# Optimization experiments

Hardware: AMD Instinct MI355X
Metric: run time of the kernel (lower is better)

## Reference

```python
import jax, jax.numpy as jnp
import numpy as np

RANK = 16
NUM_STEPS = 10
STEP_SIZE = 1000.0
INIT_SCALE = 1e-3


def _init(k, shape):
    # projection of Dirichlet-like init onto sphere neighborhood: center +- init_scale uniform noise
    center = 1.0 / np.sqrt(shape[-1])
    return (center + (2.0 * INIT_SCALE) * jax.random.uniform(k, shape, dtype=jnp.float32) - INIT_SCALE)


def setup_inputs() -> dict:
    key = jax.random.key(0)
    ks = jax.random.split(key, 5)
    B, H, S, D = 2, 12, 8192, 64
    query = jax.random.normal(ks[0], (B, H, S, D), dtype=jnp.float32)
    key_t = jax.random.normal(ks[1], (B, H, S, D), dtype=jnp.float32)
    value = jax.random.normal(ks[2], (B, H, S, D), dtype=jnp.float32)
    left_params = _init(ks[3], (B, H, S, RANK))
    right_params = _init(ks[4], (B, H, RANK, S))
    return {"query": query, "key": key_t, "value": value,
            "left_params": left_params, "right_params": right_params}


def _unit(x):
    return x / jnp.linalg.norm(x, axis=-1, keepdims=True)


def _grad(lp, rp, q, k, inv_s2):
    # lp: [..., S, r]  rp: [..., r, S]  q,k: [..., S, D]
    ls = _unit(lp)
    rs = _unit(rp)
    L = ls * ls   # left simplex factor  [..., S, r]
    R = rs * rs   # right simplex factor [..., r, S]

    # d_left = (L (R R^T) - Q (K^T R^T)) / S^2   -- contract small dims first, never SxS
    RR = jnp.einsum('...ki,...li->...kl', R, R)          # [r, r]
    KR = jnp.einsum('...ia,...li->...la', k, R)          # [r, D]
    dl = (jnp.einsum('...jk,...kl->...jl', L, RR)
          - jnp.einsum('...ja,...la->...jl', q, KR)) * inv_s2
    dl = dl * 2.0 * ls
    dl = dl - ls * jnp.sum(ls * dl, axis=-1, keepdims=True)   # tangent-space projection
    dl = dl / jnp.linalg.norm(lp, axis=-1, keepdims=True)

    # d_right = ((L^T L) R - (L^T Q) K^T) / S^2
    LL = jnp.einsum('...jk,...jl->...kl', L, L)          # [r, r]
    LQ = jnp.einsum('...jk,...ja->...ka', L, q)          # [r, D]
    dr = (jnp.einsum('...kl,...li->...ki', LL, R)
          - jnp.einsum('...ka,...ia->...ki', LQ, k)) * inv_s2
    dr = dr * 2.0 * rs
    dr = dr - rs * jnp.sum(rs * dr, axis=-1, keepdims=True)
    dr = dr / jnp.linalg.norm(rp, axis=-1, keepdims=True)
    return dl, dr


def _forward(query, key, value, left_params, right_params):
    S = query.shape[-2]
    inv_s2 = jnp.float32(1.0 / (S * S))

    def step(carry, _):
        lp, rp = carry
        dl, dr = _grad(lp, rp, query, key, inv_s2)
        return (lp - STEP_SIZE * dl, rp - STEP_SIZE * dr), None

    (lp, rp), _ = jax.lax.scan(step, (left_params, right_params), None, length=NUM_STEPS)
    left = _unit(lp) ** 2    # [..., S, r]
    right = _unit(rp) ** 2   # [..., r, S]
    # left @ (right @ value) -- rank-bottleneck multiply, O(S*r*D)
    rv = jnp.einsum('...ki,...id->...kd', right, value)
    return jnp.einsum('...jk,...kd->...jd', left, rv)


def reference(query, key, value, left_params, right_params):
    return _forward(query, key, value, left_params, right_params)
```

## Files before the change

### kernel.cpp

```cpp
#include <hip/hip_runtime.h>

#define S_ 8192
#define D_ 64
#define R_ 16
#define BH_ 24

static constexpr float INV_S2 = 1.0f / (8192.0f * 8192.0f);
static constexpr float STEPSZ = 1000.0f;
static constexpr float CC = 2.0f * INV_S2;

#define LP_N (BH_ * S_ * R_)
#define PART_STRIDE 2576
#define PART_N (BH_ * 32 * PART_STRIDE)
#define ACCF_STRIDE 2624
#define ACCF_N (BH_ * ACCF_STRIDE)
#define PART2_STRIDE 1040
#define PART2_N (BH_ * 32 * PART2_STRIDE)

__global__ void __launch_bounds__(256) kA(const float* __restrict__ lp_src,
                                          const float* __restrict__ rp_src,
                                          const float* __restrict__ q,
                                          const float* __restrict__ key,
                                          float* __restrict__ part) {
  const int bh = blockIdx.y, bx = blockIdx.x, t = threadIdx.x;
  const int tc = t & 15, trw = t >> 4, w = t >> 6;
  __shared__ float lds[6144];
  const int j0 = bx * 256;

  {
    size_t base = ((size_t)bh * S_ + j0 + t) * R_;
    const float4* s4 = (const float4*)(lp_src + base);
    float4 a0 = s4[0], a1 = s4[1], a2 = s4[2], a3 = s4[3];
    float n2 = a0.x*a0.x + a0.y*a0.y + a0.z*a0.z + a0.w*a0.w
             + a1.x*a1.x + a1.y*a1.y + a1.z*a1.z + a1.w*a1.w
             + a2.x*a2.x + a2.y*a2.y + a2.z*a2.z + a2.w*a2.w
             + a3.x*a3.x + a3.y*a3.y + a3.z*a3.z + a3.w*a3.w;
    float r2 = 1.0f / n2;
    float4* st = (float4*)(lds + t * 16);
    st[0] = make_float4(a0.x*a0.x*r2, a0.y*a0.y*r2, a0.z*a0.z*r2, a0.w*a0.w*r2);
    st[1] = make_float4(a1.x*a1.x*r2, a1.y*a1.y*r2, a1.z*a1.z*r2, a1.w*a1.w*r2);
    st[2] = make_float4(a2.x*a2.x*r2, a2.y*a2.y*r2, a2.z*a2.z*r2, a2.w*a2.w*r2);
    st[3] = make_float4(a3.x*a3.x*r2, a3.y*a3.y*r2, a3.z*a3.z*r2, a3.w*a3.w*r2);
  }
  __syncthreads();

  float acc[5][16];
#pragma unroll
  for (int u = 0; u < 5; ++u)
#pragma unroll
    for (int l = 0; l < 16; ++l) acc[u][l] = 0.f;

  const float* qb = q + (size_t)bh * S_ * D_;
  for (int it = 0; it < 16; ++it) {
    int jl = trw + (it << 4);
    const float4* L4 = (const float4*)(lds + jl * 16);
    float4 b0 = L4[0], b1 = L4[1], b2 = L4[2], b3 = L4[3];
    float Lv[16] = {b0.x, b0.y, b0.z, b0.w, b1.x, b1.y, b1.z, b1.w,
                    b2.x, b2.y, b2.z, b2.w, b3.x, b3.y, b3.z, b3.w};
    float Lc = lds[jl * 16 + tc];
    float qv[4];
#pragma unroll
    for (int u = 0; u < 4; ++u) qv[u] = qb[(size_t)(j0 + jl) * D_ + tc + (u << 4)];
#pragma unroll
    for (int u = 0; u < 4; ++u)
#pragma unroll
      for (int l = 0; l < 16; ++l) acc[u][l] += Lv[l] * qv[u];
#pragma unroll
    for (int l = 0; l < 16; ++l) acc[4][l] += Lv[l] * Lc;
  }
#pragma unroll
  for (int u = 0; u < 5; ++u)
#pragma unroll
    for (int l = 0; l < 16; ++l) {
      float v = acc[u][l];
      v += __shfl_xor(v, 16);
      v += __shfl_xor(v, 32);
      acc[u][l] = v;
    }
  __syncthreads();
  if ((t & 63) < 16) {
#pragma unroll
    for (int u = 0; u < 5; ++u)
#pragma unroll
      for (int l = 0; l < 16; ++l) lds[w * 1536 + tc * 96 + u * 16 + l] = acc[u][l];
  }
  __syncthreads();
  float* pb = part + (size_t)(bh * 32 + bx) * PART_STRIDE;
#pragma unroll
  for (int r = 0; r < 5; ++r) {
    int o = t + r * 256;
    int sl = o >> 4, c = o & 15;
    pb[o] = lds[c * 96 + sl] + lds[1536 + c * 96 + sl] +
            lds[3072 + c * 96 + sl] + lds[4608 + c * 96 + sl];
  }
  __syncthreads();

  {
    size_t cb = (size_t)bh * R_ * S_ + j0 + t;
    float* st = lds + t * 16;
#pragma unroll
    for (int l = 0; l < 16; ++l) {
      float x = rp_src[cb + (size_t)l * S_];
      st[l] = x * x;
    }
  }
  __syncthreads();

  float accN[16];
#pragma unroll
  for (int u = 0; u < 5; ++u)
#pragma unroll
    for (int l = 0; l < 16; ++l) acc[u][l] = 0.f;
#pragma unroll
  for (int l = 0; l < 16; ++l) accN[l] = 0.f;

  const float* kb = key + (size_t)bh * S_ * D_;
  for (int it = 0; it < 16; ++it) {
    int jl = trw + (it << 4);
    const float4* R4 = (const float4*)(lds + jl * 16);
    float4 b0 = R4[0], b1 = R4[1], b2 = R4[2], b3 = R4[3];
    float rv[16] = {b0.x, b0.y, b0.z, b0.w, b1.x, b1.y, b1.z, b1.w,
                    b2.x, b2.y, b2.z, b2.w, b3.x, b3.y, b3.z, b3.w};
    float rc = lds[jl * 16 + tc];
    float kv[4];
#pragma unroll
    for (int u = 0; u < 4; ++u) kv[u] = kb[(size_t)(j0 + jl) * D_ + tc + (u << 4)];
#pragma unroll
    for (int u = 0; u < 4; ++u)
#pragma unroll
      for (int l = 0; l < 16; ++l) acc[u][l] += rv[l] * kv[u];
#pragma unroll
    for (int l = 0; l < 16; ++l) acc[4][l] += rv[l] * rc;
#pragma unroll
    for (int l = 0; l < 16; ++l) accN[l] += rv[l];
  }
#pragma unroll
  for (int u = 0; u < 5; ++u)
#pragma unroll
    for (int l = 0; l < 16; ++l) {
      float v = acc[u][l];
      v += __shfl_xor(v, 16);
      v += __shfl_xor(v, 32);
      acc[u][l] = v;
    }
#pragma unroll
  for (int l = 0; l < 16; ++l) {
    float v = accN[l];
    v += __shfl_xor(v, 16);
    v += __shfl_xor(v, 32);
    accN[l] = v;
  }
  __syncthreads();
  if ((t & 63) < 16) {
#pragma unroll
    for (int u = 0; u < 5; ++u)
#pragma unroll
      for (int l = 0; l < 16; ++l) lds[w * 1536 + tc * 96 + u * 16 + l] = acc[u][l];
    if (tc == 0) {
#pragma unroll
      for (int l = 0; l < 16; ++l) lds[w * 1536 + 80 + l] = accN[l];
    }
  }
  __syncthreads();
#pragma unroll
  for (int r = 0; r < 5; ++r) {
    int o = t + r * 256;
    int sl = o >> 4, c = o & 15;
    pb[1280 + o] = lds[c * 96 + sl] + lds[1536 + c * 96 + sl] +
                   lds[3072 + c * 96 + sl] + lds[4608 + c * 96 + sl];
  }
  if (t < 16)
    pb[2560 + t] = lds[80 + t] + lds[1536 + 80 + t] + lds[3072 + 80 + t] + lds[4608 + 80 + t];
}

__global__ void __launch_bounds__(256) kB(const float* __restrict__ part,
                                          float* __restrict__ accF) {
  const int bh = blockIdx.x, t = threadIdx.x;
  __shared__ float raw[PART_STRIDE];
  __shared__ float inn[16], srn[16];
  const float* p0 = part + (size_t)bh * 32 * PART_STRIDE;
  for (int v = t; v < PART_STRIDE; v += 256) {
    float s = 0.f;
    const float* p = p0 + v;
#pragma unroll 8
    for (int b = 0; b < 32; ++b) s += p[(size_t)b * PART_STRIDE];
    raw[v] = s;
  }
  __syncthreads();
  if (t < 16) {
    float N = raw[2560 + t];
    inn[t] = 1.0f / N;
    srn[t] = rsqrtf(N);
  }
  __syncthreads();
  float* out = accF + (size_t)bh * ACCF_STRIDE;
  {
    int k = t >> 4, l = t & 15;
    float LLr = raw[(64 + k) * 16 + l];
    out[k * 16 + l] = LLr * CC * inn[l];
    float RRr = raw[1280 + (64 + k) * 16 + l];
    out[1280 + k * 16 + l] = RRr * CC * inn[k] * inn[l];
  }
#pragma unroll
  for (int r = 0; r < 4; ++r) {
    int e = t + r * 256;
    int k = e >> 6, a = e & 63, u = a >> 4, c = a & 15;
    out[256 + e] = raw[(u * 16 + k) * 16 + c] * CC;
  }
#pragma unroll
  for (int r = 0; r < 4; ++r) {
    int e = t + r * 256;
    int a = e >> 4, l = e & 15, u = a >> 4, c = a & 15;
    out[1536 + e] = raw[1280 + (u * 16 + l) * 16 + c] * CC * inn[l];
  }
  if (t < 16) {
    int k = t;
    float s = 0.f;
#pragma unroll
    for (int l = 0; l < 16; ++l)
      s += raw[(64 + k) * 16 + l] * CC * inn[l] * raw[1280 + (64 + k) * 16 + l];
#pragma unroll
    for (int a = 0; a < 64; ++a) {
      int u = a >> 4, c = a & 15;
      s -= raw[(u * 16 + k) * 16 + c] * CC * raw[1280 + (u * 16 + k) * 16 + c];
    }
    float PJ = inn[k] * s;
    out[2560 + t] = 1.0f + STEPSZ * PJ * inn[t];
    out[2576 + t] = STEPSZ * srn[t];
    out[2592 + t] = srn[t];
    out[2608 + t] = inn[t];
  }
}

template <int LAST>
__global__ void __launch_bounds__(256) kStep(const float* __restrict__ accF,
                                             const float* __restrict__ q,
                                             const float* __restrict__ key,
                                             const float* __restrict__ vv,
                                             const float* __restrict__ lp_src,
                                             const float* __restrict__ rp_src,
                                             float* __restrict__ lp_dst,
                                             float* __restrict__ rp_dst,
                                             float* __restrict__ part,
                                             float* __restrict__ part2) {
  const int bh = blockIdx.y, bx = blockIdx.x, t = threadIdx.x;
  const int tc = t & 15, trw = t >> 4, w = t >> 6;
  const int j0 = bx * 256;
  __shared__ float F[1344];
  __shared__ float lds[6144];
  const float* A = accF + (size_t)bh * ACCF_STRIDE;

  if (blockIdx.z == 0) {
    for (int e = t; e < 1280; e += 256) F[e] = A[1280 + e];
    __syncthreads();
    const float4* RR4 = (const float4*)F;
    const float4* KR4 = (const float4*)(F + 256);

    size_t base = ((size_t)bh * S_ + j0 + t) * R_;
    const float4* s4 = (const float4*)(lp_src + base);
    float4 a0 = s4[0], a1 = s4[1], a2 = s4[2], a3 = s4[3];
    float lv[16] = {a0.x, a0.y, a0.z, a0.w, a1.x, a1.y, a1.z, a1.w,
                    a2.x, a2.y, a2.z, a2.w, a3.x, a3.y, a3.z, a3.w};
    float n2 = 0.f;
#pragma unroll
    for (int l = 0; l < 16; ++l) n2 += lv[l] * lv[l];
    float ri = rsqrtf(n2);
    float ls[16], L[16];
#pragma unroll
    for (int l = 0; l < 16; ++l) { ls[l] = lv[l] * ri; L[l] = ls[l] * ls[l]; }
    float dl[16];
#pragma unroll
    for (int l = 0; l < 16; ++l) dl[l] = 0.f;
#pragma unroll
    for (int k = 0; k < 16; ++k) {
      float Lk = L[k];
#pragma unroll
      for (int g = 0; g < 4; ++g) {
        float4 rr = RR4[k * 4 + g];
        dl[4 * g + 0] += Lk * rr.x; dl[4 * g + 1] += Lk * rr.y;
        dl[4 * g + 2] += Lk * rr.z; dl[4 * g + 3] += Lk * rr.w;
      }
    }
    const float4* q4 = (const float4*)(q + ((size_t)bh * S_ + j0 + t) * D_);
#pragma unroll
    for (int a4 = 0; a4 < 16; ++a4) {
      float4 qq = q4[a4];
#pragma unroll
      for (int c = 0; c < 4; ++c) {
        float qa = (c == 0) ? qq.x : (c == 1) ? qq.y : (c == 2) ? qq.z : qq.w;
        int a = a4 * 4 + c;
#pragma unroll
        for (int g = 0; g < 4; ++g) {
          float4 kr = KR4[a * 4 + g];
          dl[4 * g + 0] -= qa * kr.x; dl[4 * g + 1] -= qa * kr.y;
          dl[4 * g + 2] -= qa * kr.z; dl[4 * g + 3] -= qa * kr.w;
        }
      }
    }
    float dot = 0.f;
#pragma unroll
    for (int l = 0; l < 16; ++l) { dl[l] *= ls[l]; dot += ls[l] * dl[l]; }
#pragma unroll
    for (int l = 0; l < 16; ++l)
      lv[l] -= STEPSZ * (dl[l] - ls[l] * dot) * ri;
    float4* d4 = (float4*)(lp_dst + base);
    d4[0] = make_float4(lv[0], lv[1], lv[2], lv[3]);
    d4[1] = make_float4(lv[4], lv[5], lv[6], lv[7]);
    d4[2] = make_float4(lv[8], lv[9], lv[10], lv[11]);
    d4[3] = make_float4(lv[12], lv[13], lv[14], lv[15]);

    if (LAST) return;

    float m2 = 0.f;
#pragma unroll
    for (int l = 0; l < 16; ++l) m2 += lv[l] * lv[l];
    float r2 = 1.0f / m2;
    {
      float4* st = (float4*)(lds + t * 16);
      st[0] = make_float4(lv[0]*lv[0]*r2, lv[1]*lv[1]*r2, lv[2]*lv[2]*r2, lv[3]*lv[3]*r2);
      st[1] = make_float4(lv[4]*lv[4]*r2, lv[5]*lv[5]*r2, lv[6]*lv[6]*r2, lv[7]*lv[7]*r2);
      st[2] = make_float4(lv[8]*lv[8]*r2, lv[9]*lv[9]*r2, lv[10]*lv[10]*r2, lv[11]*lv[11]*r2);
      st[3] = make_float4(lv[12]*lv[12]*r2, lv[13]*lv[13]*r2, lv[14]*lv[14]*r2, lv[15]*lv[15]*r2);
    }
    __syncthreads();
    float acc[5][16];
#pragma unroll
    for (int u = 0; u < 5; ++u)
#pragma unroll
      for (int l = 0; l < 16; ++l) acc[u][l] = 0.f;
    const float* qb = q + (size_t)bh * S_ * D_;
    for (int it = 0; it < 16; ++it) {
      int jl = trw + (it << 4);
      const float4* L4 = (const float4*)(lds + jl * 16);
      float4 b0 = L4[0], b1 = L4[1], b2 = L4[2], b3 = L4[3];
      float Lv[16] = {b0.x, b0.y, b0.z, b0.w, b1.x, b1.y, b1.z, b1.w,
                      b2.x, b2.y, b2.z, b2.w, b3.x, b3.y, b3.z, b3.w};
      float Lc = lds[jl * 16 + tc];
      float qv[4];
#pragma unroll
      for (int u = 0; u < 4; ++u) qv[u] = qb[(size_t)(j0 + jl) * D_ + tc + (u << 4)];
#pragma unroll
      for (int u = 0; u < 4; ++u)
#pragma unroll
        for (int l = 0; l < 16; ++l) acc[u][l] += Lv[l] * qv[u];
#pragma unroll
      for (int l = 0; l < 16; ++l) acc[4][l] += Lv[l] * Lc;
    }
#pragma unroll
    for (int u = 0; u < 5; ++u)
#pragma unroll
      for (int l = 0; l < 16; ++l) {
        float v = acc[u][l];
        v += __shfl_xor(v, 16);
        v += __shfl_xor(v, 32);
        acc[u][l] = v;
      }
    __syncthreads();
    if ((t & 63) < 16) {
#pragma unroll
      for (int u = 0; u < 5; ++u)
#pragma unroll
        for (int l = 0; l < 16; ++l) lds[w * 1536 + tc * 96 + u * 16 + l] = acc[u][l];
    }
    __syncthreads();
    float* pb = part + (size_t)(bh * 32 + bx) * PART_STRIDE;
#pragma unroll
    for (int r = 0; r < 5; ++r) {
      int o = t + r * 256;
      int sl = o >> 4, c = o & 15;
      pb[o] = lds[c * 96 + sl] + lds[1536 + c * 96 + sl] +
              lds[3072 + c * 96 + sl] + lds[4608 + c * 96 + sl];
    }
  } else {
    for (int e = t; e < 1328; e += 256) F[e] = (e < 1280) ? A[e] : A[1280 + e];
    __syncthreads();
    const float4* MLL4 = (const float4*)F;
    const float4* MLQ4 = (const float4*)(F + 256);
    const float* C1 = F + 1280;
    const float* C2 = F + 1296;
    const float* SRN = F + 1312;

    const int i = j0 + t;
    size_t cbase = (size_t)bh * R_ * S_ + i;
    float rv[16], rp2[16];
#pragma unroll
    for (int l = 0; l < 16; ++l) {
      float x = rp_src[cbase + (size_t)l * S_];
      rv[l] = x;
      rp2[l] = x * x;
    }
    float s[16];
#pragma unroll
    for (int k = 0; k < 16; ++k) {
      float acc0 = 0.f;
#pragma unroll
      for (int g = 0; g < 4; ++g) {
        float4 m = MLL4[k * 4 + g];
        acc0 += m.x * rp2[4 * g + 0] + m.y * rp2[4 * g + 1] +
                m.z * rp2[4 * g + 2] + m.w * rp2[4 * g + 3];
      }
      s[k] = acc0;
    }
    const float4* k4 = (const float4*)(key + ((size_t)bh * S_ + i) * D_);
#pragma unroll
    for (int a4 = 0; a4 < 16; ++a4) {
      float4 kk = k4[a4];
#pragma unroll
      for (int k = 0; k < 16; ++k) {
        float4 m = MLQ4[k * 16 + a4];
        s[k] -= m.x * kk.x + m.y * kk.y + m.z * kk.z + m.w * kk.w;
      }
    }
#pragma unroll
    for (int k = 0; k < 16; ++k) {
      float rs = rv[k] * SRN[k];
      float d2 = rs * s[k];
      float nv = C1[k] * rv[k] - C2[k] * d2;
      rp_dst[cbase + (size_t)k * S_] = nv;
      rp2[k] = nv * nv;
    }
    {
      float* st = lds + t * 16;
#pragma unroll
      for (int l = 0; l < 16; ++l) st[l] = rp2[l];
    }
    __syncthreads();
    float acc[5][16], accN[16];
#pragma unroll
    for (int u = 0; u < 5; ++u)
#pragma unroll
      for (int l = 0; l < 16; ++l) acc[u][l] = 0.f;
#pragma unroll
    for (int l = 0; l < 16; ++l) accN[l] = 0.f;
    const float* sb = (LAST ? vv : key) + (size_t)bh * S_ * D_;
    for (int it = 0; it < 16; ++it) {
      int jl = trw + (it << 4);
      const float4* R4 = (const float4*)(lds + jl * 16);
      float4 b0 = R4[0], b1 = R4[1], b2 = R4[2], b3 = R4[3];
      float rw[16] = {b0.x, b0.y, b0.z, b0.w, b1.x, b1.y, b1.z, b1.w,
                      b2.x, b2.y, b2.z, b2.w, b3.x, b3.y, b3.z, b3.w};
      float rc = lds[jl * 16 + tc];
      float kv[4];
#pragma unroll
      for (int u = 0; u < 4; ++u) kv[u] = sb[(size_t)(j0 + jl) * D_ + tc + (u << 4)];
#pragma unroll
      for (int u = 0; u < 4; ++u)
#pragma unroll
        for (int l = 0; l < 16; ++l) acc[u][l] += rw[l] * kv[u];
#pragma unroll
      for (int l = 0; l < 16; ++l) acc[4][l] += rw[l] * rc;
#pragma unroll
      for (int l = 0; l < 16; ++l) accN[l] += rw[l];
    }
#pragma unroll
    for (int u = 0; u < 5; ++u)
#pragma unroll
      for (int l = 0; l < 16; ++l) {
        float v = acc[u][l];
        v += __shfl_xor(v, 16);
        v += __shfl_xor(v, 32);
        acc[u][l] = v;
      }
#pragma unroll
    for (int l = 0; l < 16; ++l) {
      float v = accN[l];
      v += __shfl_xor(v, 16);
      v += __shfl_xor(v, 32);
      accN[l] = v;
    }
    __syncthreads();
    if ((t & 63) < 16) {
#pragma unroll
      for (int u = 0; u < 5; ++u)
#pragma unroll
        for (int l = 0; l < 16; ++l) lds[w * 1536 + tc * 96 + u * 16 + l] = acc[u][l];
      if (tc == 0) {
#pragma unroll
        for (int l = 0; l < 16; ++l) lds[w * 1536 + 80 + l] = accN[l];
      }
    }
    __syncthreads();
    if (!LAST) {
      float* pb = part + (size_t)(bh * 32 + bx) * PART_STRIDE;
#pragma unroll
      for (int r = 0; r < 5; ++r) {
        int o = t + r * 256;
        int sl = o >> 4, c = o & 15;
        pb[1280 + o] = lds[c * 96 + sl] + lds[1536 + c * 96 + sl] +
                       lds[3072 + c * 96 + sl] + lds[4608 + c * 96 + sl];
      }
      if (t < 16)
        pb[2560 + t] = lds[80 + t] + lds[1536 + 80 + t] + lds[3072 + 80 + t] + lds[4608 + 80 + t];
    } else {
      float* pb2 = part2 + (size_t)(bh * 32 + bx) * PART2_STRIDE;
#pragma unroll
      for (int r = 0; r < 4; ++r) {
        int o = t + r * 256;
        int sl = o >> 4, c = o & 15;
        pb2[o] = lds[c * 96 + sl] + lds[1536 + c * 96 + sl] +
                 lds[3072 + c * 96 + sl] + lds[4608 + c * 96 + sl];
      }
      if (t < 16)
        pb2[1024 + t] = lds[80 + t] + lds[1536 + 80 + t] + lds[3072 + 80 + t] + lds[4608 + 80 + t];
    }
  }
}

__global__ void __launch_bounds__(256) kBF(const float* __restrict__ part2,
                                           float* __restrict__ RVs) {
  const int bh = blockIdx.x, t = threadIdx.x;
  __shared__ float raw[PART2_STRIDE];
  __shared__ float inn[16];
  const float* p0 = part2 + (size_t)bh * 32 * PART2_STRIDE;
  for (int v = t; v < PART2_STRIDE; v += 256) {
    float s = 0.f;
    const float* p = p0 + v;
#pragma unroll 8
    for (int b = 0; b < 32; ++b) s += p[(size_t)b * PART2_STRIDE];
    raw[v] = s;
  }
  __syncthreads();
  if (t < 16) inn[t] = 1.0f / raw[1024 + t];
  __syncthreads();
#pragma unroll
  for (int r = 0; r < 4; ++r) {
    int e = t + r * 256;
    int k = e >> 6, d = e & 63, u = d >> 4, c = d & 15;
    RVs[(size_t)bh * 1024 + e] = raw[(u * 16 + k) * 16 + c] * inn[k];
  }
}

__global__ void __launch_bounds__(256) kOut(const float* __restrict__ lp,
                                            const float* __restrict__ RVs,
                                            float* __restrict__ out) {
  const int bh = blockIdx.y, t = threadIdx.x;
  __shared__ float rvs[1024];
#pragma unroll
  for (int r = 0; r < 4; ++r) rvs[t + r * 256] = RVs[(size_t)bh * 1024 + t + r * 256];
  __syncthreads();
  const int j = blockIdx.x * 256 + t;
  size_t base = ((size_t)bh * S_ + j) * R_;
  const float4* lp4 = (const float4*)(lp + base);
  float4 a0 = lp4[0], a1 = lp4[1], a2 = lp4[2], a3 = lp4[3];
  float lv[16] = {a0.x, a0.y, a0.z, a0.w, a1.x, a1.y, a1.z, a1.w,
                  a2.x, a2.y, a2.z, a2.w, a3.x, a3.y, a3.z, a3.w};
  float n2 = 0.f;
#pragma unroll
  for (int l = 0; l < 16; ++l) n2 += lv[l] * lv[l];
  float r2 = 1.0f / n2;
  float L[16];
#pragma unroll
  for (int l = 0; l < 16; ++l) L[l] = lv[l] * lv[l] * r2;
  float o[64];
#pragma unroll
  for (int d = 0; d < 64; ++d) o[d] = 0.f;
  const float4* rv4 = (const float4*)rvs;
#pragma unroll
  for (int k = 0; k < 16; ++k) {
    float Lk = L[k];
#pragma unroll
    for (int d4 = 0; d4 < 16; ++d4) {
      float4 r = rv4[k * 16 + d4];
      o[4 * d4 + 0] += Lk * r.x; o[4 * d4 + 1] += Lk * r.y;
      o[4 * d4 + 2] += Lk * r.z; o[4 * d4 + 3] += Lk * r.w;
    }
  }
  float4* o4 = (float4*)(out + ((size_t)bh * S_ + j) * D_);
#pragma unroll
  for (int d4 = 0; d4 < 16; ++d4)
    o4[d4] = make_float4(o[4 * d4 + 0], o[4 * d4 + 1], o[4 * d4 + 2], o[4 * d4 + 3]);
}

extern "C" void kernel_launch(void* const* d_in, const int* in_sizes, int n_in,
                              void* d_out, int out_size, void* d_ws, size_t ws_size,
                              hipStream_t stream) {
  (void)in_sizes; (void)n_in; (void)out_size; (void)ws_size;
  const float* q = (const float*)d_in[0];
  const float* key = (const float*)d_in[1];
  const float* v = (const float*)d_in[2];
  const float* lp0 = (const float*)d_in[3];
  const float* rp0 = (const float*)d_in[4];
  float* out = (float*)d_out;
  float* ws = (float*)d_ws;

  float* lp = ws;
  float* rp = lp + LP_N;
  float* part = rp + LP_N;
  float* accF = part + PART_N;
  float* part2 = accF + ACCF_N;
  float* RVs = part2 + PART2_N;

  dim3 blk(256);
  dim3 gA(32, BH_);
  dim3 gS(32, BH_, 2);
  kA<<<gA, blk, 0, stream>>>(lp0, rp0, q, key, part);
  for (int s = 0; s < 10; ++s) {
    kB<<<dim3(BH_), blk, 0, stream>>>(part, accF);
    const float* lsrc = (s == 0) ? lp0 : lp;
    const float* rsrc = (s == 0) ? rp0 : rp;
    if (s < 9)
      kStep<0><<<gS, blk, 0, stream>>>(accF, q, key, v, lsrc, rsrc, lp, rp, part, part2);
    else
      kStep<1><<<gS, blk, 0, stream>>>(accF, q, key, v, lsrc, rsrc, lp, rp, part, part2);
  }
  kBF<<<dim3(BH_), blk, 0, stream>>>(part2, RVs);
  kOut<<<gA, blk, 0, stream>>>(lp, RVs, out);
}
```

Before: 957.4 us.

## Store right factor row-major per position and vectorize Q/K loads in step kernel

Folds the initial accumulation kernel into a templated step kernel (mode 0 copies inputs into the workspace) and switches the working right-parameter buffer from [r, S] to a per-position [S, r] layout. Each thread can then load and store its 16 rank values as float4s instead of 16 strided scalar accesses. Q/K/V tiles are now read as one float4 per thread instead of four scalar loads, and the partial-sum layouts in LDS and global memory are reindexed to match. The final step skips the RR accumulation it does not need. In exchange, per-thread accumulator register pressure rises and the reduction indexing becomes more intricate.

```diff
diff --git a/kernel.cpp b/kernel.cpp
--- a/kernel.cpp
+++ b/kernel.cpp
@@ -17,160 +17,333 @@
 #define PART2_STRIDE 1040
 #define PART2_N (BH_ * 32 * PART2_STRIDE)
 
-__global__ void __launch_bounds__(256) kA(const float* __restrict__ lp_src,
-                                          const float* __restrict__ rp_src,
-                                          const float* __restrict__ q,
-                                          const float* __restrict__ key,
-                                          float* __restrict__ part) {
+template <int MODE>
+__global__ void __launch_bounds__(256) kStep(const float* __restrict__ accF,
+                                             const float* __restrict__ q,
+                                             const float* __restrict__ key,
+                                             const float* __restrict__ vv,
+                                             const float* __restrict__ lp_src,
+                                             const float* __restrict__ rp_src,
+                                             float* __restrict__ lp_dst,
+                                             float* __restrict__ rp_dst,
+                                             float* __restrict__ part,
+                                             float* __restrict__ part2) {
   const int bh = blockIdx.y, bx = blockIdx.x, t = threadIdx.x;
-  const int tc = t & 15, trw = t >> 4, w = t >> 6;
-  __shared__ float lds[6144];
+  const int tc = t & 15, trw = t >> 4, w = t >> 6, lane = t & 63;
   const int j0 = bx * 256;
-
-  {
-    size_t base = ((size_t)bh * S_ + j0 + t) * R_;
-    const float4* s4 = (const float4*)(lp_src + base);
-    float4 a0 = s4[0], a1 = s4[1], a2 = s4[2], a3 = s4[3];
-    float n2 = a0.x*a0.x + a0.y*a0.y + a0.z*a0.z + a0.w*a0.w
-             + a1.x*a1.x + a1.y*a1.y + a1.z*a1.z + a1.w*a1.w
-             + a2.x*a2.x + a2.y*a2.y + a2.z*a2.z + a2.w*a2.w
-             + a3.x*a3.x + a3.y*a3.y + a3.z*a3.z + a3.w*a3.w;
-    float r2 = 1.0f / n2;
-    float4* st = (float4*)(lds + t * 16);
-    st[0] = make_float4(a0.x*a0.x*r2, a0.y*a0.y*r2, a0.z*a0.z*r2, a0.w*a0.w*r2);
-    st[1] = make_float4(a1.x*a1.x*r2, a1.y*a1.y*r2, a1.z*a1.z*r2, a1.w*a1.w*r2);
-    st[2] = make_float4(a2.x*a2.x*r2, a2.y*a2.y*r2, a2.z*a2.z*r2, a2.w*a2.w*r2);
-    st[3] = make_float4(a3.x*a3.x*r2, a3.y*a3.y*r2, a3.z*a3.z*r2, a3.w*a3.w*r2);
-  }
-  __syncthreads();
-
-  float acc[5][16];
-#pragma unroll
-  for (int u = 0; u < 5; ++u)
-#pragma unroll
-    for (int l = 0; l < 16; ++l) acc[u][l] = 0.f;
-
-  const float* qb = q + (size_t)bh * S_ * D_;
-  for (int it = 0; it < 16; ++it) {
-    int jl = trw + (it << 4);
-    const float4* L4 = (const float4*)(lds + jl * 16);
-    float4 b0 = L4[0], b1 = L4[1], b2 = L4[2], b3 = L4[3];
-    float Lv[16] = {b0.x, b0.y, b0.z, b0.w, b1.x, b1.y, b1.z, b1.w,
-                    b2.x, b2.y, b2.z, b2.w, b3.x, b3.y, b3.z, b3.w};
-    float Lc = lds[jl * 16 + tc];
-    float qv[4];
-#pragma unroll
-    for (int u = 0; u < 4; ++u) qv[u] = qb[(size_t)(j0 + jl) * D_ + tc + (u << 4)];
-#pragma unroll
-    for (int u = 0; u < 4; ++u)
-#pragma unroll
-      for (int l = 0; l < 16; ++l) acc[u][l] += Lv[l] * qv[u];
-#pragma unroll
-    for (int l = 0; l < 16; ++l) acc[4][l] += Lv[l] * Lc;
-  }
-#pragma unroll
-  for (int u = 0; u < 5; ++u)
+  __shared__ float B[6400];
+  const float* A = accF + (size_t)bh * ACCF_STRIDE;
+
+  if (blockIdx.z == 0) {
+    const size_t base = ((size_t)bh * S_ + j0 + t) * R_;
+    float lv[16];
+    if (MODE >= 1) {
+      for (int e = t; e < 1280; e += 256) B[e] = A[1280 + e];
+      __syncthreads();
+      const float4* RR4 = (const float4*)B;
+      const float4* KR4 = (const float4*)(B + 256);
+      const float4* s4 = (const float4*)(lp_src + base);
+      float4 a0 = s4[0], a1 = s4[1], a2 = s4[2], a3 = s4[3];
+      lv[0]=a0.x; lv[1]=a0.y; lv[2]=a0.z; lv[3]=a0.w;
+      lv[4]=a1.x; lv[5]=a1.y; lv[6]=a1.z; lv[7]=a1.w;
+      lv[8]=a2.x; lv[9]=a2.y; lv[10]=a2.z; lv[11]=a2.w;
+      lv[12]=a3.x; lv[13]=a3.y; lv[14]=a3.z; lv[15]=a3.w;
+      float n2 = 0.f;
+#pragma unroll
+      for (int l = 0; l < 16; ++l) n2 += lv[l] * lv[l];
+      float ri = rsqrtf(n2);
+      float ls[16], L[16];
+#pragma unroll
+      for (int l = 0; l < 16; ++l) { ls[l] = lv[l] * ri; L[l] = ls[l] * ls[l]; }
+      float dl[16];
+#pragma unroll
+      for (int l = 0; l < 16; ++l) dl[l] = 0.f;
+#pragma unroll
+      for (int k = 0; k < 16; ++k) {
+        float Lk = L[k];
+#pragma unroll
+        for (int g = 0; g < 4; ++g) {
+          float4 rr = RR4[k * 4 + g];
+          dl[4*g+0] += Lk * rr.x; dl[4*g+1] += Lk * rr.y;
+          dl[4*g+2] += Lk * rr.z; dl[4*g+3] += Lk * rr.w;
+        }
+      }
+      const float4* q4 = (const float4*)(q + ((size_t)bh * S_ + j0 + t) * D_);
+#pragma unroll
+      for (int a4 = 0; a4 < 16; ++a4) {
+        float4 qq = q4[a4];
+#pragma unroll
+        for (int c = 0; c < 4; ++c) {
+          float qa = (c == 0) ? qq.x : (c == 1) ? qq.y : (c == 2) ? qq.z : qq.w;
+          int a = a4 * 4 + c;
+#pragma unroll
+          for (int g = 0; g < 4; ++g) {
+            float4 kr = KR4[a * 4 + g];
+            dl[4*g+0] -= qa * kr.x; dl[4*g+1] -= qa * kr.y;
+            dl[4*g+2] -= qa * kr.z; dl[4*g+3] -= qa * kr.w;
+          }
+        }
+      }
+      float dot = 0.f;
+#pragma unroll
+      for (int l = 0; l < 16; ++l) { dl[l] *= ls[l]; dot += ls[l] * dl[l]; }
+#pragma unroll
+      for (int l = 0; l < 16; ++l) lv[l] -= STEPSZ * (dl[l] - ls[l] * dot) * ri;
+      float4* d4 = (float4*)(lp_dst + base);
+      d4[0] = make_float4(lv[0], lv[1], lv[2], lv[3]);
+      d4[1] = make_float4(lv[4], lv[5], lv[6], lv[7]);
+      d4[2] = make_float4(lv[8], lv[9], lv[10], lv[11]);
+      d4[3] = make_float4(lv[12], lv[13], lv[14], lv[15]);
+      if (MODE == 2) return;
+      __syncthreads();
+    } else {
+      const float4* s4 = (const float4*)(lp_src + base);
+      float4 a0 = s4[0], a1 = s4[1], a2 = s4[2], a3 = s4[3];
+      lv[0]=a0.x; lv[1]=a0.y; lv[2]=a0.z; lv[3]=a0.w;
+      lv[4]=a1.x; lv[5]=a1.y; lv[6]=a1.z; lv[7]=a1.w;
+      lv[8]=a2.x; lv[9]=a2.y; lv[10]=a2.z; lv[11]=a2.w;
+      lv[12]=a3.x; lv[13]=a3.y; lv[14]=a3.z; lv[15]=a3.w;
+      float4* d4 = (float4*)(lp_dst + base);
+      d4[0] = a0; d4[1] = a1; d4[2] = a2; d4[3] = a3;
+    }
+    {
+      float m2 = 0.f;
+#pragma unroll
+      for (int l = 0; l < 16; ++l) m2 += lv[l] * lv[l];
+      float r2 = 1.0f / m2;
+      float4* st = (float4*)(B + t * 16);
+      st[0] = make_float4(lv[0]*lv[0]*r2, lv[1]*lv[1]*r2, lv[2]*lv[2]*r2, lv[3]*lv[3]*r2);
+      st[1] = make_float4(lv[4]*lv[4]*r2, lv[5]*lv[5]*r2, lv[6]*lv[6]*r2, lv[7]*lv[7]*r2);
+      st[2] = make_float4(lv[8]*lv[8]*r2, lv[9]*lv[9]*r2, lv[10]*lv[10]*r2, lv[11]*lv[11]*r2);
+      st[3] = make_float4(lv[12]*lv[12]*r2, lv[13]*lv[13]*r2, lv[14]*lv[14]*r2, lv[15]*lv[15]*r2);
+    }
+    __syncthreads();
+    float aQ[64], aL[16];
+#pragma unroll
+    for (int e = 0; e < 64; ++e) aQ[e] = 0.f;
+#pragma unroll
+    for (int l = 0; l < 16; ++l) aL[l] = 0.f;
+    const float* qb = q + (size_t)bh * S_ * D_;
+    for (int it = 0; it < 16; ++it) {
+      int jl = trw + (it << 4);
+      const float4* Lw = (const float4*)(B + jl * 16);
+      float4 b0 = Lw[0], b1 = Lw[1], b2 = Lw[2], b3 = Lw[3];
+      float Lv[16] = {b0.x,b0.y,b0.z,b0.w, b1.x,b1.y,b1.z,b1.w,
+                      b2.x,b2.y,b2.z,b2.w, b3.x,b3.y,b3.z,b3.w};
+      float Lc = B[jl * 16 + tc];
+      float4 qq = *(const float4*)(qb + (size_t)(j0 + jl) * D_ + (tc << 2));
+#pragma unroll
+      for (int l = 0; l < 16; ++l) {
+        aQ[l*4+0] += Lv[l] * qq.x; aQ[l*4+1] += Lv[l] * qq.y;
+        aQ[l*4+2] += Lv[l] * qq.z; aQ[l*4+3] += Lv[l] * qq.w;
+        aL[l] += Lv[l] * Lc;
+      }
+    }
+#pragma unroll
+    for (int e = 0; e < 64; ++e) {
+      float v = aQ[e];
+      v += __shfl_xor(v, 16); v += __shfl_xor(v, 32);
+      aQ[e] = v;
+    }
 #pragma unroll
     for (int l = 0; l < 16; ++l) {
-      float v = acc[u][l];
-      v += __shfl_xor(v, 16);
-      v += __shfl_xor(v, 32);
-      acc[u][l] = v;
-    }
-  __syncthreads();
-  if ((t & 63) < 16) {
-#pragma unroll
-    for (int u = 0; u < 5; ++u)
-#pragma unroll
-      for (int l = 0; l < 16; ++l) lds[w * 1536 + tc * 96 + u * 16 + l] = acc[u][l];
-  }
-  __syncthreads();
-  float* pb = part + (size_t)(bh * 32 + bx) * PART_STRIDE;
-#pragma unroll
-  for (int r = 0; r < 5; ++r) {
-    int o = t + r * 256;
-    int sl = o >> 4, c = o & 15;
-    pb[o] = lds[c * 96 + sl] + lds[1536 + c * 96 + sl] +
-            lds[3072 + c * 96 + sl] + lds[4608 + c * 96 + sl];
-  }
-  __syncthreads();
-
-  {
-    size_t cb = (size_t)bh * R_ * S_ + j0 + t;
-    float* st = lds + t * 16;
+      float v = aL[l];
+      v += __shfl_xor(v, 16); v += __shfl_xor(v, 32);
+      aL[l] = v;
+    }
+    __syncthreads();
+    if (lane < 16) {
+      float* rg = B + w * 1600 + tc * 100;
+      float4* rg4 = (float4*)rg;
+#pragma unroll
+      for (int l = 0; l < 16; ++l)
+        rg4[l] = make_float4(aQ[l*4], aQ[l*4+1], aQ[l*4+2], aQ[l*4+3]);
+#pragma unroll
+      for (int l = 0; l < 16; ++l) rg[64 + l] = aL[l];
+    }
+    __syncthreads();
+    float* pb = part + (size_t)(bh * 32 + bx) * PART_STRIDE;
+#pragma unroll
+    for (int r = 0; r < 4; ++r) {
+      int o = t + r * 256;
+      int tcL = o >> 6, sl = o & 63;
+      int idx = tcL * 100 + sl;
+      float s = B[idx] + B[idx + 1600] + B[idx + 3200] + B[idx + 4800];
+      pb[((tcL << 2) + (sl & 3)) * 16 + (sl >> 2)] = s;
+    }
+    {
+      int tcL = t >> 4, l = t & 15;
+      int idx = tcL * 100 + 64 + l;
+      float s = B[idx] + B[idx + 1600] + B[idx + 3200] + B[idx + 4800];
+      pb[1024 + l * 16 + tcL] = s;
+    }
+  } else {
+    const int i = j0 + t;
+    const size_t cb = ((size_t)bh * S_ + i) * R_;
+    float nv[16], rp2[16];
+    if (MODE >= 1) {
+      for (int e = t; e < 1328; e += 256) B[e] = (e < 1280) ? A[e] : A[1280 + e];
+      __syncthreads();
+      const float4* MLL4 = (const float4*)B;
+      const float4* MLQ4 = (const float4*)(B + 256);
+      const float* C1 = B + 1280;
+      const float* C2 = B + 1296;
+      const float* SRN = B + 1312;
+      const float4* r4 = (const float4*)(rp_src + cb);
+      float4 a0 = r4[0], a1 = r4[1], a2 = r4[2], a3 = r4[3];
+      float rv[16] = {a0.x,a0.y,a0.z,a0.w, a1.x,a1.y,a1.z,a1.w,
+                      a2.x,a2.y,a2.z,a2.w, a3.x,a3.y,a3.z,a3.w};
+#pragma unroll
+      for (int l = 0; l < 16; ++l) rp2[l] = rv[l] * rv[l];
+      float s[16];
+#pragma unroll
+      for (int k = 0; k < 16; ++k) {
+        float acc0 = 0.f;
+#pragma unroll
+        for (int g = 0; g < 4; ++g) {
+          float4 m = MLL4[k * 4 + g];
+          acc0 += m.x * rp2[4*g+0] + m.y * rp2[4*g+1] +
+                  m.z * rp2[4*g+2] + m.w * rp2[4*g+3];
+        }
+        s[k] = acc0;
+      }
+      const float4* k4 = (const float4*)(key + ((size_t)bh * S_ + i) * D_);
+#pragma unroll
+      for (int a4 = 0; a4 < 16; ++a4) {
+        float4 kk = k4[a4];
+#pragma unroll
+        for (int k = 0; k < 16; ++k) {
+          float4 m = MLQ4[k * 16 + a4];
+          s[k] -= m.x * kk.x + m.y * kk.y + m.z * kk.z + m.w * kk.w;
+        }
+      }
+#pragma unroll
+      for (int k = 0; k < 16; ++k) {
+        float rs = rv[k] * SRN[k];
+        float d2 = rs * s[k];
+        nv[k] = C1[k] * rv[k] - C2[k] * d2;
+        rp2[k] = nv[k] * nv[k];
+      }
+      float4* d4 = (float4*)(rp_dst + cb);
+      d4[0] = make_float4(nv[0], nv[1], nv[2], nv[3]);
+      d4[1] = make_float4(nv[4], nv[5], nv[6], nv[7]);
+      d4[2] = make_float4(nv[8], nv[9], nv[10], nv[11]);
+      d4[3] = make_float4(nv[12], nv[13], nv[14], nv[15]);
+      __syncthreads();
+    } else {
+      const float* rsrc = rp_src + (size_t)bh * R_ * S_ + i;
+#pragma unroll
+      for (int k = 0; k < 16; ++k) {
+        float x = rsrc[(size_t)k * S_];
+        nv[k] = x;
+        rp2[k] = x * x;
+      }
+      float4* d4 = (float4*)(rp_dst + cb);
+      d4[0] = make_float4(nv[0], nv[1], nv[2], nv[3]);
+      d4[1] = make_float4(nv[4], nv[5], nv[6], nv[7]);
+      d4[2] = make_float4(nv[8], nv[9], nv[10], nv[11]);
+      d4[3] = make_float4(nv[12], nv[13], nv[14], nv[15]);
+    }
+    {
+      float4* st = (float4*)(B + t * 16);
+      st[0] = make_float4(rp2[0], rp2[1], rp2[2], rp2[3]);
+      st[1] = make_float4(rp2[4], rp2[5], rp2[6], rp2[7]);
+      st[2] = make_float4(rp2[8], rp2[9], rp2[10], rp2[11]);
+      st[3] = make_float4(rp2[12], rp2[13], rp2[14], rp2[15]);
+    }
+    __syncthreads();
+    float aQ[64], aR[16], aN[16];
+#pragma unroll
+    for (int e = 0; e < 64; ++e) aQ[e] = 0.f;
+#pragma unroll
+    for (int l = 0; l < 16; ++l) { aR[l] = 0.f; aN[l] = 0.f; }
+    const float* sb = ((MODE == 2) ? vv : key) + (size_t)bh * S_ * D_;
+    for (int it = 0; it < 16; ++it) {
+      int jl = trw + (it << 4);
+      const float4* Rw = (const float4*)(B + jl * 16);
+      float4 b0 = Rw[0], b1 = Rw[1], b2 = Rw[2], b3 = Rw[3];
+      float rw[16] = {b0.x,b0.y,b0.z,b0.w, b1.x,b1.y,b1.z,b1.w,
+                      b2.x,b2.y,b2.z,b2.w, b3.x,b3.y,b3.z,b3.w};
+      float rc = (MODE < 2) ? B[jl * 16 + tc] : 0.f;
+      float4 kk = *(const float4*)(sb + (size_t)(j0 + jl) * D_ + (tc << 2));
+#pragma unroll
+      for (int l = 0; l < 16; ++l) {
+        aQ[l*4+0] += rw[l] * kk.x; aQ[l*4+1] += rw[l] * kk.y;
+        aQ[l*4+2] += rw[l] * kk.z; aQ[l*4+3] += rw[l] * kk.w;
+        if (MODE < 2) aR[l] += rw[l] * rc;
+        aN[l] += rw[l];
+      }
+    }
+#pragma unroll
+    for (int e = 0; e < 64; ++e) {
+      float v = aQ[e];
+      v += __shfl_xor(v, 16); v += __shfl_xor(v, 32);
+      aQ[e] = v;
+    }
 #pragma unroll
     for (int l = 0; l < 16; ++l) {
-      float x = rp_src[cb + (size_t)l * S_];
-      st[l] = x * x;
-    }
-  }
-  __syncthreads();
-
-  float accN[16];
-#pragma unroll
-  for (int u = 0; u < 5; ++u)
-#pragma unroll
-    for (int l = 0; l < 16; ++l) acc[u][l] = 0.f;
-#pragma unroll
-  for (int l = 0; l < 16; ++l) accN[l] = 0.f;
-
-  const float* kb = key + (size_t)bh * S_ * D_;
-  for (int it = 0; it < 16; ++it) {
-    int jl = trw + (it << 4);
-    const float4* R4 = (const float4*)(lds + jl * 16);
-    float4 b0 = R4[0], b1 = R4[1], b2 = R4[2], b3 = R4[3];
-    float rv[16] = {b0.x, b0.y, b0.z, b0.w, b1.x, b1.y, b1.z, b1.w,
-                    b2.x, b2.y, b2.z, b2.w, b3.x, b3.y, b3.z, b3.w};
-    float rc = lds[jl * 16 + tc];
-    float kv[4];
-#pragma unroll
-    for (int u = 0; u < 4; ++u) kv[u] = kb[(size_t)(j0 + jl) * D_ + tc + (u << 4)];
-#pragma unroll
-    for (int u = 0; u < 4; ++u)
-#pragma unroll
-      for (int l = 0; l < 16; ++l) acc[u][l] += rv[l] * kv[u];
-#pragma unroll
-    for (int l = 0; l < 16; ++l) acc[4][l] += rv[l] * rc;
-#pragma unroll
-    for (int l = 0; l < 16; ++l) accN[l] += rv[l];
-  }
-#pragma unroll
-  for (int u = 0; u < 5; ++u)
-#pragma unroll
-    for (int l = 0; l < 16; ++l) {
-      float v = acc[u][l];
-      v += __shfl_xor(v, 16);
-      v += __shfl_xor(v, 32);
-      acc[u][l] = v;
-    }
-#pragma unroll
-  for (int l = 0; l < 16; ++l) {
-    float v = accN[l];
-    v += __shfl_xor(v, 16);
-    v += __shfl_xor(v, 32);
-    accN[l] = v;
-  }
-  __syncthreads();
-  if ((t & 63) < 16) {
-#pragma unroll
-    for (int u = 0; u < 5; ++u)
-#pragma unroll
-      for (int l = 0; l < 16; ++l) lds[w * 1536 + tc * 96 + u * 16 + l] = acc[u][l];
-    if (tc == 0) {
-#pragma unroll
-      for (int l = 0; l < 16; ++l) lds[w * 1536 + 80 + l] = accN[l];
-    }
-  }
-  __syncthreads();
-#pragma unroll
-  for (int r = 0; r < 5; ++r) {
-    int o = t + r * 256;
-    int sl = o >> 4, c = o & 15;
-    pb[1280 + o] = lds[c * 96 + sl] + lds[1536 + c * 96 + sl] +
-                   lds[3072 + c * 96 + sl] + lds[4608 + c * 96 + sl];
-  }
-  if (t < 16)
-    pb[2560 + t] = lds[80 + t] + lds[1536 + 80 + t] + lds[3072 + 80 + t] + lds[4608 + 80 + t];
+      float v = aN[l];
+      v += __shfl_xor(v, 16); v += __shfl_xor(v, 32);
+      aN[l] = v;
+      if (MODE < 2) {
+        float u = aR[l];
+        u += __shfl_xor(u, 16); u += __shfl_xor(u, 32);
+        aR[l] = u;
+      }
+    }
+    __syncthreads();
+    if (lane < 16) {
+      float* rg = B + w * 1600 + tc * 100;
+      float4* rg4 = (float4*)rg;
+#pragma unroll
+      for (int l = 0; l < 16; ++l)
+        rg4[l] = make_float4(aQ[l*4], aQ[l*4+1], aQ[l*4+2], aQ[l*4+3]);
+      if (MODE < 2) {
+#pragma unroll
+        for (int l = 0; l < 16; ++l) rg[64 + l] = aR[l];
+      }
+    }
+    if (lane == 0) {
+#pragma unroll
+      for (int l = 0; l < 16; ++l) B[w * 1600 + 80 + l] = aN[l];
+    }
+    __syncthreads();
+    if (MODE < 2) {
+      float* pb = part + (size_t)(bh * 32 + bx) * PART_STRIDE + 1280;
+#pragma unroll
+      for (int r = 0; r < 4; ++r) {
+        int o = t + r * 256;
+        int tcL = o >> 6, sl = o & 63;
+        int idx = tcL * 100 + sl;
+        float s = B[idx] + B[idx + 1600] + B[idx + 3200] + B[idx + 4800];
+        pb[((tcL << 2) + (sl & 3)) * 16 + (sl >> 2)] = s;
+      }
+      {
+        int tcL = t >> 4, l = t & 15;
+        int idx = tcL * 100 + 64 + l;
+        float s = B[idx] + B[idx + 1600] + B[idx + 3200] + B[idx + 4800];
+        pb[1024 + l * 16 + tcL] = s;
+      }
+      if (t < 16) {
+        int idx = 80 + t;
+        pb[1280 + t] = B[idx] + B[idx + 1600] + B[idx + 3200] + B[idx + 4800];
+      }
+    } else {
+      float* pb2 = part2 + (size_t)(bh * 32 + bx) * PART2_STRIDE;
+#pragma unroll
+      for (int r = 0; r < 4; ++r) {
+        int o = t + r * 256;
+        int tcL = o >> 6, sl = o & 63;
+        int idx = tcL * 100 + sl;
+        float s = B[idx] + B[idx + 1600] + B[idx + 3200] + B[idx + 4800];
+        pb2[((tcL << 2) + (sl & 3)) * 16 + (sl >> 2)] = s;
+      }
+      if (t < 16) {
+        int idx = 80 + t;
+        pb2[1024 + t] = B[idx] + B[idx + 1600] + B[idx + 3200] + B[idx + 4800];
+      }
+    }
+  }
 }
 
 __global__ void __launch_bounds__(256) kB(const float* __restrict__ part,
@@ -194,315 +367,32 @@
   }
   __syncthreads();
   float* out = accF + (size_t)bh * ACCF_STRIDE;
-  {
-    int k = t >> 4, l = t & 15;
-    float LLr = raw[(64 + k) * 16 + l];
-    out[k * 16 + l] = LLr * CC * inn[l];
-    float RRr = raw[1280 + (64 + k) * 16 + l];
-    out[1280 + k * 16 + l] = RRr * CC * inn[k] * inn[l];
-  }
+  out[t] = raw[1024 + t] * CC * inn[t & 15];
+  out[1280 + t] = raw[2304 + t] * CC * inn[t >> 4] * inn[t & 15];
 #pragma unroll
   for (int r = 0; r < 4; ++r) {
     int e = t + r * 256;
-    int k = e >> 6, a = e & 63, u = a >> 4, c = a & 15;
-    out[256 + e] = raw[(u * 16 + k) * 16 + c] * CC;
+    out[256 + e] = raw[((e & 63) << 4) + (e >> 6)] * CC;
   }
 #pragma unroll
   for (int r = 0; r < 4; ++r) {
     int e = t + r * 256;
-    int a = e >> 4, l = e & 15, u = a >> 4, c = a & 15;
-    out[1536 + e] = raw[1280 + (u * 16 + l) * 16 + c] * CC * inn[l];
+    out[1536 + e] = raw[1280 + e] * CC * inn[e & 15];
   }
   if (t < 16) {
     int k = t;
     float s = 0.f;
 #pragma unroll
     for (int l = 0; l < 16; ++l)
-      s += raw[(64 + k) * 16 + l] * CC * inn[l] * raw[1280 + (64 + k) * 16 + l];
-#pragma unroll
-    for (int a = 0; a < 64; ++a) {
-      int u = a >> 4, c = a & 15;
-      s -= raw[(u * 16 + k) * 16 + c] * CC * raw[1280 + (u * 16 + k) * 16 + c];
-    }
+      s += raw[1024 + k * 16 + l] * CC * inn[l] * raw[2304 + k * 16 + l];
+#pragma unroll
+    for (int a = 0; a < 64; ++a)
+      s -= raw[a * 16 + k] * CC * raw[1280 + a * 16 + k];
     float PJ = inn[k] * s;
     out[2560 + t] = 1.0f + STEPSZ * PJ * inn[t];
     out[2576 + t] = STEPSZ * srn[t];
     out[2592 + t] = srn[t];
     out[2608 + t] = inn[t];
-  }
-}
-
-template <int LAST>
-__global__ void __launch_bounds__(256) kStep(const float* __restrict__ accF,
-                                             const float* __restrict__ q,
-                                             const float* __restrict__ key,
-                                             const float* __restrict__ vv,
-                                             const float* __restrict__ lp_src,
-                                             const float* __restrict__ rp_src,
-                                             float* __restrict__ lp_dst,
-                                             float* __restrict__ rp_dst,
-                                             float* __restrict__ part,
-                                             float* __restrict__ part2) {
-  const int bh = blockIdx.y, bx = blockIdx.x, t = threadIdx.x;
-  const int tc = t & 15, trw = t >> 4, w = t >> 6;
-  const int j0 = bx * 256;
-  __shared__ float F[1344];
-  __shared__ float lds[6144];
-  const float* A = accF + (size_t)bh * ACCF_STRIDE;
-
-  if (blockIdx.z == 0) {
-    for (int e = t; e < 1280; e += 256) F[e] = A[1280 + e];
-    __syncthreads();
-    const float4* RR4 = (const float4*)F;
-    const float4* KR4 = (const float4*)(F + 256);
-
-    size_t base = ((size_t)bh * S_ + j0 + t) * R_;
-    const float4* s4 = (const float4*)(lp_src + base);
-    float4 a0 = s4[0], a1 = s4[1], a2 = s4[2], a3 = s4[3];
-    float lv[16] = {a0.x, a0.y, a0.z, a0.w, a1.x, a1.y, a1.z, a1.w,
-                    a2.x, a2.y, a2.z, a2.w, a3.x, a3.y, a3.z, a3.w};
-    float n2 = 0.f;
-#pragma unroll
-    for (int l = 0; l < 16; ++l) n2 += lv[l] * lv[l];
-    float ri = rsqrtf(n2);
-    float ls[16], L[16];
-#pragma unroll
-    for (int l = 0; l < 16; ++l) { ls[l] = lv[l] * ri; L[l] = ls[l] * ls[l]; }
-    float dl[16];
-#pragma unroll
-    for (int l = 0; l < 16; ++l) dl[l] = 0.f;
-#pragma unroll
-    for (int k = 0; k < 16; ++k) {
-      float Lk = L[k];
-#pragma unroll
-      for (int g = 0; g < 4; ++g) {
-        float4 rr = RR4[k * 4 + g];
-        dl[4 * g + 0] += Lk * rr.x; dl[4 * g + 1] += Lk * rr.y;
-        dl[4 * g + 2] += Lk * rr.z; dl[4 * g + 3] += Lk * rr.w;
-      }
-    }
-    const float4* q4 = (const float4*)(q + ((size_t)bh * S_ + j0 + t) * D_);
-#pragma unroll
-    for (int a4 = 0; a4 < 16; ++a4) {
-      float4 qq = q4[a4];
-#pragma unroll
-      for (int c = 0; c < 4; ++c) {
-        float qa = (c == 0) ? qq.x : (c == 1) ? qq.y : (c == 2) ? qq.z : qq.w;
-        int a = a4 * 4 + c;
-#pragma unroll
-        for (int g = 0; g < 4; ++g) {
-          float4 kr = KR4[a * 4 + g];
-          dl[4 * g + 0] -= qa * kr.x; dl[4 * g + 1] -= qa * kr.y;
-          dl[4 * g + 2] -= qa * kr.z; dl[4 * g + 3] -= qa * kr.w;
-        }
-      }
-    }
-    float dot = 0.f;
-#pragma unroll
-    for (int l = 0; l < 16; ++l) { dl[l] *= ls[l]; dot += ls[l] * dl[l]; }
-#pragma unroll
-    for (int l = 0; l < 16; ++l)
-      lv[l] -= STEPSZ * (dl[l] - ls[l] * dot) * ri;
-    float4* d4 = (float4*)(lp_dst + base);
-    d4[0] = make_float4(lv[0], lv[1], lv[2], lv[3]);
-    d4[1] = make_float4(lv[4], lv[5], lv[6], lv[7]);
-    d4[2] = make_float4(lv[8], lv[9], lv[10], lv[11]);
-    d4[3] = make_float4(lv[12], lv[13], lv[14], lv[15]);
-
-    if (LAST) return;
-
-    float m2 = 0.f;
-#pragma unroll
-    for (int l = 0; l < 16; ++l) m2 += lv[l] * lv[l];
-    float r2 = 1.0f / m2;
-    {
-      float4* st = (float4*)(lds + t * 16);
-      st[0] = make_float4(lv[0]*lv[0]*r2, lv[1]*lv[1]*r2, lv[2]*lv[2]*r2, lv[3]*lv[3]*r2);
-      st[1] = make_float4(lv[4]*lv[4]*r2, lv[5]*lv[5]*r2, lv[6]*lv[6]*r2, lv[7]*lv[7]*r2);
-      st[2] = make_float4(lv[8]*lv[8]*r2, lv[9]*lv[9]*r2, lv[10]*lv[10]*r2, lv[11]*lv[11]*r2);
-      st[3] = make_float4(lv[12]*lv[12]*r2, lv[13]*lv[13]*r2, lv[14]*lv[14]*r2, lv[15]*lv[15]*r2);
-    }
-    __syncthreads();
-    float acc[5][16];
-#pragma unroll
-    for (int u = 0; u < 5; ++u)
-#pragma unroll
-      for (int l = 0; l < 16; ++l) acc[u][l] = 0.f;
-    const float* qb = q + (size_t)bh * S_ * D_;
-    for (int it = 0; it < 16; ++it) {
-      int jl = trw + (it << 4);
-      const float4* L4 = (const float4*)(lds + jl * 16);
-      float4 b0 = L4[0], b1 = L4[1], b2 = L4[2], b3 = L4[3];
-      float Lv[16] = {b0.x, b0.y, b0.z, b0.w, b1.x, b1.y, b1.z, b1.w,
-                      b2.x, b2.y, b2.z, b2.w, b3.x, b3.y, b3.z, b3.w};
-      float Lc = lds[jl * 16 + tc];
-      float qv[4];
-#pragma unroll
-      for (int u = 0; u < 4; ++u) qv[u] = qb[(size_t)(j0 + jl) * D_ + tc + (u << 4)];
-#pragma unroll
-      for (int u = 0; u < 4; ++u)
-#pragma unroll
-        for (int l = 0; l < 16; ++l) acc[u][l] += Lv[l] * qv[u];
-#pragma unroll
-      for (int l = 0; l < 16; ++l) acc[4][l] += Lv[l] * Lc;
-    }
-#pragma unroll
-    for (int u = 0; u < 5; ++u)
-#pragma unroll
-      for (int l = 0; l < 16; ++l) {
-        float v = acc[u][l];
-        v += __shfl_xor(v, 16);
-        v += __shfl_xor(v, 32);
-        acc[u][l] = v;
-      }
-    __syncthreads();
-    if ((t & 63) < 16) {
-#pragma unroll
-      for (int u = 0; u < 5; ++u)
-#pragma unroll
-        for (int l = 0; l < 16; ++l) lds[w * 1536 + tc * 96 + u * 16 + l] = acc[u][l];
-    }
-    __syncthreads();
-    float* pb = part + (size_t)(bh * 32 + bx) * PART_STRIDE;
-#pragma unroll
-    for (int r = 0; r < 5; ++r) {
-      int o = t + r * 256;
-      int sl = o >> 4, c = o & 15;
-      pb[o] = lds[c * 96 + sl] + lds[1536 + c * 96 + sl] +
-              lds[3072 + c * 96 + sl] + lds[4608 + c * 96 + sl];
-    }
-  } else {
-    for (int e = t; e < 1328; e += 256) F[e] = (e < 1280) ? A[e] : A[1280 + e];
-    __syncthreads();
-    const float4* MLL4 = (const float4*)F;
-    const float4* MLQ4 = (const float4*)(F + 256);
-    const float* C1 = F + 1280;
-    const float* C2 = F + 1296;
-    const float* SRN = F + 1312;
-
-    const int i = j0 + t;
-    size_t cbase = (size_t)bh * R_ * S_ + i;
-    float rv[16], rp2[16];
-#pragma unroll
-    for (int l = 0; l < 16; ++l) {
-      float x = rp_src[cbase + (size_t)l * S_];
-      rv[l] = x;
-      rp2[l] = x * x;
-    }
-    float s[16];
-#pragma unroll
-    for (int k = 0; k < 16; ++k) {
-      float acc0 = 0.f;
-#pragma unroll
-      for (int g = 0; g < 4; ++g) {
-        float4 m = MLL4[k * 4 + g];
-        acc0 += m.x * rp2[4 * g + 0] + m.y * rp2[4 * g + 1] +
-                m.z * rp2[4 * g + 2] + m.w * rp2[4 * g + 3];
-      }
-      s[k] = acc0;
-    }
-    const float4* k4 = (const float4*)(key + ((size_t)bh * S_ + i) * D_);
-#pragma unroll
-    for (int a4 = 0; a4 < 16; ++a4) {
-      float4 kk = k4[a4];
-#pragma unroll
-      for (int k = 0; k < 16; ++k) {
-        float4 m = MLQ4[k * 16 + a4];
-        s[k] -= m.x * kk.x + m.y * kk.y + m.z * kk.z + m.w * kk.w;
-      }
-    }
-#pragma unroll
-    for (int k = 0; k < 16; ++k) {
-      float rs = rv[k] * SRN[k];
-      float d2 = rs * s[k];
-      float nv = C1[k] * rv[k] - C2[k] * d2;
-      rp_dst[cbase + (size_t)k * S_] = nv;
-      rp2[k] = nv * nv;
-    }
-    {
-      float* st = lds + t * 16;
-#pragma unroll
-      for (int l = 0; l < 16; ++l) st[l] = rp2[l];
-    }
-    __syncthreads();
-    float acc[5][16], accN[16];
-#pragma unroll
-    for (int u = 0; u < 5; ++u)
-#pragma unroll
-      for (int l = 0; l < 16; ++l) acc[u][l] = 0.f;
-#pragma unroll
-    for (int l = 0; l < 16; ++l) accN[l] = 0.f;
-    const float* sb = (LAST ? vv : key) + (size_t)bh * S_ * D_;
-    for (int it = 0; it < 16; ++it) {
-      int jl = trw + (it << 4);
-      const float4* R4 = (const float4*)(lds + jl * 16);
-      float4 b0 = R4[0], b1 = R4[1], b2 = R4[2], b3 = R4[3];
-      float rw[16] = {b0.x, b0.y, b0.z, b0.w, b1.x, b1.y, b1.z, b1.w,
-                      b2.x, b2.y, b2.z, b2.w, b3.x, b3.y, b3.z, b3.w};
-      float rc = lds[jl * 16 + tc];
-      float kv[4];
-#pragma unroll
-      for (int u = 0; u < 4; ++u) kv[u] = sb[(size_t)(j0 + jl) * D_ + tc + (u << 4)];
-#pragma unroll
-      for (int u = 0; u < 4; ++u)
-#pragma unroll
-        for (int l = 0; l < 16; ++l) acc[u][l] += rw[l] * kv[u];
-#pragma unroll
-      for (int l = 0; l < 16; ++l) acc[4][l] += rw[l] * rc;
-#pragma unroll
-      for (int l = 0; l < 16; ++l) accN[l] += rw[l];
-    }
-#pragma unroll
-    for (int u = 0; u < 5; ++u)
-#pragma unroll
-      for (int l = 0; l < 16; ++l) {
-        float v = acc[u][l];
-        v += __shfl_xor(v, 16);
-        v += __shfl_xor(v, 32);
-        acc[u][l] = v;
-      }
-#pragma unroll
-    for (int l = 0; l < 16; ++l) {
-      float v = accN[l];
-      v += __shfl_xor(v, 16);
-      v += __shfl_xor(v, 32);
-      accN[l] = v;
-    }
-    __syncthreads();
-    if ((t & 63) < 16) {
-#pragma unroll
-      for (int u = 0; u < 5; ++u)
-#pragma unroll
-        for (int l = 0; l < 16; ++l) lds[w * 1536 + tc * 96 + u * 16 + l] = acc[u][l];
-      if (tc == 0) {
-#pragma unroll
-        for (int l = 0; l < 16; ++l) lds[w * 1536 + 80 + l] = accN[l];
-      }
-    }
-    __syncthreads();
-    if (!LAST) {
-      float* pb = part + (size_t)(bh * 32 + bx) * PART_STRIDE;
-#pragma unroll
-      for (int r = 0; r < 5; ++r) {
-        int o = t + r * 256;
-        int sl = o >> 4, c = o & 15;
-        pb[1280 + o] = lds[c * 96 + sl] + lds[1536 + c * 96 + sl] +
-                       lds[3072 + c * 96 + sl] + lds[4608 + c * 96 + sl];
-      }
-      if (t < 16)
-        pb[2560 + t] = lds[80 + t] + lds[1536 + 80 + t] + lds[3072 + 80 + t] + lds[4608 + 80 + t];
-    } else {
-      float* pb2 = part2 + (size_t)(bh * 32 + bx) * PART2_STRIDE;
-#pragma unroll
-      for (int r = 0; r < 4; ++r) {
-        int o = t + r * 256;
-        int sl = o >> 4, c = o & 15;
-        pb2[o] = lds[c * 96 + sl] + lds[1536 + c * 96 + sl] +
-                 lds[3072 + c * 96 + sl] + lds[4608 + c * 96 + sl];
-      }
-      if (t < 16)
-        pb2[1024 + t] = lds[80 + t] + lds[1536 + 80 + t] + lds[3072 + 80 + t] + lds[4608 + 80 + t];
-    }
   }
 }
 
@@ -525,8 +415,7 @@
 #pragma unroll
   for (int r = 0; r < 4; ++r) {
     int e = t + r * 256;
-    int k = e >> 6, d = e & 63, u = d >> 4, c = d & 15;
-    RVs[(size_t)bh * 1024 + e] = raw[(u * 16 + k) * 16 + c] * inn[k];
+    RVs[(size_t)bh * 1024 + e] = raw[((e & 63) << 4) + (e >> 6)] * inn[e >> 6];
   }
 }
 
@@ -542,8 +431,8 @@
   size_t base = ((size_t)bh * S_ + j) * R_;
   const float4* lp4 = (const float4*)(lp + base);
   float4 a0 = lp4[0], a1 = lp4[1], a2 = lp4[2], a3 = lp4[3];
-  float lv[16] = {a0.x, a0.y, a0.z, a0.w, a1.x, a1.y, a1.z, a1.w,
-                  a2.x, a2.y, a2.z, a2.w, a3.x, a3.y, a3.z, a3.w};
+  float lv[16] = {a0.x,a0.y,a0.z,a0.w, a1.x,a1.y,a1.z,a1.w,
+                  a2.x,a2.y,a2.z,a2.w, a3.x,a3.y,a3.z,a3.w};
   float n2 = 0.f;
 #pragma unroll
   for (int l = 0; l < 16; ++l) n2 += lv[l] * lv[l];
@@ -561,14 +450,14 @@
 #pragma unroll
     for (int d4 = 0; d4 < 16; ++d4) {
       float4 r = rv4[k * 16 + d4];
-      o[4 * d4 + 0] += Lk * r.x; o[4 * d4 + 1] += Lk * r.y;
-      o[4 * d4 + 2] += Lk * r.z; o[4 * d4 + 3] += Lk * r.w;
+      o[4*d4+0] += Lk * r.x; o[4*d4+1] += Lk * r.y;
+      o[4*d4+2] += Lk * r.z; o[4*d4+3] += Lk * r.w;
     }
   }
   float4* o4 = (float4*)(out + ((size_t)bh * S_ + j) * D_);
 #pragma unroll
   for (int d4 = 0; d4 < 16; ++d4)
-    o4[d4] = make_float4(o[4 * d4 + 0], o[4 * d4 + 1], o[4 * d4 + 2], o[4 * d4 + 3]);
+    o4[d4] = make_float4(o[4*d4+0], o[4*d4+1], o[4*d4+2], o[4*d4+3]);
 }
 
 extern "C" void kernel_launch(void* const* d_in, const int* in_sizes, int n_in,
@@ -591,18 +480,15 @@
   float* RVs = part2 + PART2_N;
 
   dim3 blk(256);
-  dim3 gA(32, BH_);
   dim3 gS(32, BH_, 2);
-  kA<<<gA, blk, 0, stream>>>(lp0, rp0, q, key, part);
+  kStep<0><<<gS, blk, 0, stream>>>(accF, q, key, v, lp0, rp0, lp, rp, part, part2);
   for (int s = 0; s < 10; ++s) {
     kB<<<dim3(BH_), blk, 0, stream>>>(part, accF);
-    const float* lsrc = (s == 0) ? lp0 : lp;
-    const float* rsrc = (s == 0) ? rp0 : rp;
     if (s < 9)
-      kStep<0><<<gS, blk, 0, stream>>>(accF, q, key, v, lsrc, rsrc, lp, rp, part, part2);
+      kStep<1><<<gS, blk, 0, stream>>>(accF, q, key, v, lp, rp, lp, rp, part, part2);
     else
-      kStep<1><<<gS, blk, 0, stream>>>(accF, q, key, v, lsrc, rsrc, lp, rp, part, part2);
+      kStep<2><<<gS, blk, 0, stream>>>(accF, q, key, v, lp, rp, lp, rp, part, part2);
   }
   kBF<<<dim3(BH_), blk, 0, stream>>>(part2, RVs);
-  kOut<<<gA, blk, 0, stream>>>(lp, RVs, out);
+  kOut<<<dim3(32, BH_), blk, 0, stream>>>(lp, RVs, out);
 }
```

Result: faster. 933.0 us (-2.5%).
